# Kernel optimization log

Hardware: AMD Instinct MI355X
Metric: run time of the kernel (lower is better)

## Reference

```python
import jax, jax.numpy as jnp
import numpy as np
import itertools

# The repo's eset_ops_4_to_4 builds 69 permutation-equivariant basis ops on a
# rank-4 set tensor x[n, d, i, j, k, l]. We reconstruct the 69-dim basis as all
# order-preserving subset matchings (A, B) with A = kept input index slots,
# B = output slots receiving them (|A| = |B| = s, s = 1..4): sum x over the
# complement of A, then broadcast the reduced tensor into output positions B.
# Count: sum_{s=1..4} C(4,s)^2 = 16 + 36 + 16 + 1 = 69 (Vandermonde C(8,4)=70
# minus the s=0 global-sum term).

def _basis_pairs():
    pairs = []
    for s in range(1, 5):
        for A in itertools.combinations(range(4), s):
            for B in itertools.combinations(range(4), s):
                pairs.append((A, B))
    return pairs  # len == 69

_PAIRS = _basis_pairs()


def _forward(x, coefs, bias):
    # x: (n, d, N, N, N, N); coefs: (d, s_out, 69); bias: (1, s_out, 1,1,1,1)
    out_shape = (x.shape[0], coefs.shape[1]) + x.shape[2:]
    out = jnp.zeros(out_shape, x.dtype)
    for idx, (A, B) in enumerate(_PAIRS):
        sum_axes = tuple(2 + i for i in range(4) if i not in A)
        red = x.sum(axis=sum_axes) if sum_axes else x  # (n, d, N^|A|)
        # mix channels on the SMALL reduced tensor (op and channel mix commute)
        term = jnp.einsum('ds,nd...->ns...', coefs[:, :, idx], red)
        # place kept axes at output slots B (order-preserving), broadcast rest
        for p in range(4):
            if p not in B:
                term = jnp.expand_dims(term, axis=2 + p)
        out = out + term  # broadcasting add == broadcast then accumulate
    return out + bias


def setup_inputs() -> dict:
    key = jax.random.key(0)
    k1, k2 = jax.random.split(key)
    n, d, s_out, N, basis = 2, 8, 8, 32, 69
    x = jax.random.normal(k1, (n, d, N, N, N, N), dtype=jnp.float32)
    std = np.sqrt(2.0 / (d + s_out + basis)).astype(np.float32)
    coefs = std * jax.random.normal(k2, (d, s_out, basis), dtype=jnp.float32)
    bias = jnp.zeros((1, s_out, 1, 1, 1, 1), dtype=jnp.float32)
    return {'x': x, 'coefs': coefs, 'bias': bias}


def reference(x, coefs, bias):
    return _forward(x, coefs, bias)
```

## Files before the change

### kernel.cpp

```cpp
#include <hip/hip_runtime.h>


constexpr size_t R3SZ  = 524288;
constexpr size_t R2SZ  = 16384;
constexpr size_t R1SZ  = 512;
constexpr size_t R3OFF = 0;
constexpr size_t R2OFF = R3OFF + 4 * R3SZ;
constexpr size_t R1OFF = R2OFF + 6 * R2SZ;
constexpr size_t T2OFF = R1OFF + 4 * R1SZ;
constexpr size_t T1OFF = T2OFF + 6 * R2SZ;
constexpr size_t U3OFF = T1OFF + 4 * R1SZ;

__global__ __launch_bounds__(256) void k_plane(const float* __restrict__ x,
                                               float* __restrict__ ws) {
    __shared__ float4 cp[4][8];
    __shared__ float b012[256];
    __shared__ float b013[256];
    const int bid = blockIdx.x;
    const int jq = bid & 3;
    const int i  = (bid >> 2) & 31;
    const int nd = bid >> 7;
    const int t  = threadIdx.x;
    const int w  = t >> 6;
    const int lane = t & 63;
    const float* xp = x + ((size_t)nd << 20) + ((size_t)i << 15) + (size_t)jq * 8192;

    #pragma unroll
    for (int jj = 0; jj < 8; ++jj) {
        float4 v = *(const float4*)(xp + jj * 1024 + t * 4);
        float h = v.x + v.y + v.z + v.w;
        h += __shfl_xor(h, 1); h += __shfl_xor(h, 2); h += __shfl_xor(h, 4);
        if ((t & 7) == 0) b012[jj * 32 + (t >> 3)] = h;
        v.x += __shfl_xor(v.x, 8);  v.y += __shfl_xor(v.y, 8);
        v.z += __shfl_xor(v.z, 8);  v.w += __shfl_xor(v.w, 8);
        v.x += __shfl_xor(v.x, 16); v.y += __shfl_xor(v.y, 16);
        v.z += __shfl_xor(v.z, 16); v.w += __shfl_xor(v.w, 16);
        v.x += __shfl_xor(v.x, 32); v.y += __shfl_xor(v.y, 32);
        v.z += __shfl_xor(v.z, 32); v.w += __shfl_xor(v.w, 32);
        if (lane < 8) cp[w][lane] = v;
        __syncthreads();
        if (t < 8) {
            float4 s0 = cp[0][t], s1 = cp[1][t], s2 = cp[2][t], s3 = cp[3][t];
            float4 s;
            s.x = s0.x + s1.x + s2.x + s3.x;
            s.y = s0.y + s1.y + s2.y + s3.y;
            s.z = s0.z + s1.z + s2.z + s3.z;
            s.w = s0.w + s1.w + s2.w + s3.w;
            *(float4*)(&b013[jj * 32 + t * 4]) = s;
        }
        __syncthreads();
    }
    const size_t base = ((size_t)nd << 15) + ((size_t)i << 10) + jq * 256;
    ws[R3OFF + base + t]         = b012[t];
    ws[R3OFF + R3SZ + base + t]  = b013[t];
}

__global__ __launch_bounds__(256) void k_col(const float* __restrict__ x,
                                             float* __restrict__ ws) {
    const int b = blockIdx.x;
    const int t = threadIdx.x;
    if (b < 512) {
        const int i  = b & 31;
        const int nd = b >> 5;
        const float* xp = x + ((size_t)nd << 20) + ((size_t)i << 15) + t * 4;
        float4 acc = {0.f, 0.f, 0.f, 0.f};
        #pragma unroll 8
        for (int j = 0; j < 32; ++j) {
            float4 v = *(const float4*)(xp + j * 1024);
            acc.x += v.x; acc.y += v.y; acc.z += v.z; acc.w += v.w;
        }
        *(float4*)(ws + R3OFF + 2 * R3SZ + ((size_t)nd << 15) + ((size_t)i << 10)
                   + t * 4) = acc;
    } else {
        const int bb = b - 512;
        const int j  = bb & 31;
        const int nd = bb >> 5;
        const float* xp = x + ((size_t)nd << 20) + (size_t)j * 1024 + t * 4;
        float4 acc = {0.f, 0.f, 0.f, 0.f};
        #pragma unroll 8
        for (int i = 0; i < 32; ++i) {
            float4 v = *(const float4*)(xp + ((size_t)i << 15));
            acc.x += v.x; acc.y += v.y; acc.z += v.z; acc.w += v.w;
        }
        *(float4*)(ws + R3OFF + 3 * R3SZ + ((size_t)nd << 15) + ((size_t)j << 10)
                   + t * 4) = acc;
    }
}

__global__ __launch_bounds__(256) void k_red21(float* __restrict__ ws) {
    const int gid = blockIdx.x * 256 + threadIdx.x;
    if (gid < 98304) {
        const int b2 = gid >> 14;
        const int r  = gid & 16383;
        const int nd = r >> 10;
        const int p = (r >> 5) & 31, q = r & 31;
        const float* r012 = ws + R3OFF + ((size_t)nd << 15);
        const float* r013 = r012 + R3SZ;
        const float* r023 = r012 + 2 * R3SZ;
        float s = 0.f;
        switch (b2) {
            case 0: { const float* s0 = r012 + p * 1024 + q * 32;
                      for (int m = 0; m < 32; ++m) s += s0[m]; } break;
            case 1: { const float* s0 = r012 + p * 1024 + q;
                      for (int m = 0; m < 32; ++m) s += s0[m * 32]; } break;
            case 2: { const float* s0 = r013 + p * 1024 + q;
                      for (int m = 0; m < 32; ++m) s += s0[m * 32]; } break;
            case 3: { const float* s0 = r012 + p * 32 + q;
                      for (int m = 0; m < 32; ++m) s += s0[m * 1024]; } break;
            case 4: { const float* s0 = r013 + p * 32 + q;
                      for (int m = 0; m < 32; ++m) s += s0[m * 1024]; } break;
            default:{ const float* s0 = r023 + p * 32 + q;
                      for (int m = 0; m < 32; ++m) s += s0[m * 1024]; } break;
        }
        ws[R2OFF + (size_t)b2 * R2SZ + (size_t)nd * 1024 + p * 32 + q] = s;
    } else if (gid < 100352) {
        const int e  = gid - 98304;
        const int b1 = e >> 9;
        const int r  = e & 511;
        const int nd = r >> 5, p = r & 31;
        const float* r012 = ws + R3OFF + ((size_t)nd << 15);
        const float* r013 = r012 + R3SZ;
        float s = 0.f;
        if (b1 == 0)      { const float* s0 = r012 + p * 1024;
                            for (int m = 0; m < 1024; ++m) s += s0[m]; }
        else if (b1 == 1) { const float* s0 = r012 + p * 32;
                            for (int a = 0; a < 32; ++a) for (int m = 0; m < 32; ++m)
                                s += s0[a * 1024 + m]; }
        else if (b1 == 2) { const float* s0 = r012 + p;
                            for (int a = 0; a < 32; ++a) for (int m = 0; m < 32; ++m)
                                s += s0[a * 1024 + m * 32]; }
        else              { const float* s0 = r013 + p;
                            for (int a = 0; a < 32; ++a) for (int m = 0; m < 32; ++m)
                                s += s0[a * 1024 + m * 32]; }
        ws[R1OFF + (size_t)b1 * R1SZ + (size_t)nd * 32 + p] = s;
    }
}

__global__ __launch_bounds__(256) void k_mix21(const float* __restrict__ coefs,
                                               float* __restrict__ ws) {
    __shared__ float cs[4416];
    for (int idx = threadIdx.x; idx < 4416; idx += 256) cs[idx] = coefs[idx];
    __syncthreads();
    const int gid = blockIdx.x * 256 + threadIdx.x;
    if (gid < 98304) {
        const int b2 = gid >> 14;
        const int r  = gid & 16383;
        const int n  = r >> 13;
        const int so = (r >> 10) & 7;
        const int pq = r & 1023;
        float s = 0.f;
        #pragma unroll
        for (int a2 = 0; a2 < 6; ++a2) {
            const float* src = ws + R2OFF + (size_t)a2 * R2SZ + (size_t)(n * 8) * 1024 + pq;
            #pragma unroll
            for (int d = 0; d < 8; ++d)
                s += cs[(d * 8 + so) * 69 + 16 + a2 * 6 + b2] * src[d * 1024];
        }
        ws[T2OFF + (size_t)b2 * R2SZ + (size_t)(n * 8 + so) * 1024 + pq] = s;
    } else if (gid < 100352) {
        const int e  = gid - 98304;
        const int b1 = e >> 9;
        const int r  = e & 511;
        const int n  = r >> 8;
        const int so = (r >> 5) & 7;
        const int p  = r & 31;
        float s = 0.f;
        #pragma unroll
        for (int a1 = 0; a1 < 4; ++a1) {
            const float* src = ws + R1OFF + (size_t)a1 * R1SZ + (size_t)(n * 8) * 32 + p;
            #pragma unroll
            for (int d = 0; d < 8; ++d)
                s += cs[(d * 8 + so) * 69 + a1 * 4 + b1] * src[d * 32];
        }
        ws[T1OFF + (size_t)b1 * R1SZ + (size_t)(n * 8 + so) * 32 + p] = s;
    }
}

__global__ __launch_bounds__(256) void k_mix3(const float* __restrict__ coefs,
                                              const float* __restrict__ bias,
                                              float* __restrict__ ws) {
    __shared__ float cs[4416];
    for (int idx = threadIdx.x; idx < 4416; idx += 256) cs[idx] = coefs[idx];
    __syncthreads();
    const int blk = blockIdx.x;
    const int cb  = blk & 127;
    const int soh = (blk >> 7) & 1;
    const int n   = blk >> 8;
    const int c   = cb * 256 + threadIdx.x;
    const int p1 = c >> 10, p2 = (c >> 5) & 31, p3 = c & 31;
    float v[4][8];
    #pragma unroll
    for (int a = 0; a < 4; ++a)
        #pragma unroll
        for (int d = 0; d < 8; ++d)
            v[a][d] = ws[R3OFF + (size_t)a * R3SZ + (size_t)(n * 8 + d) * 32768 + c];
    const float* T2 = ws + T2OFF;
    const float* T1 = ws + T1OFF;
    #pragma unroll
    for (int b = 0; b < 4; ++b) {
        #pragma unroll
        for (int so2 = 0; so2 < 4; ++so2) {
            const int so = soh * 4 + so2;
            float s = 0.f;
            #pragma unroll
            for (int a = 0; a < 4; ++a)
                #pragma unroll
                for (int d = 0; d < 8; ++d)
                    s += cs[(d * 8 + so) * 69 + 52 + a * 4 + b] * v[a][d];
            const size_t nso = (size_t)(n * 8 + so);
            if (b == 0) {
                s += T2[0 * R2SZ + nso * 1024 + p1 * 32 + p2];
                s += T2[1 * R2SZ + nso * 1024 + p1 * 32 + p3];
                s += T2[3 * R2SZ + nso * 1024 + p2 * 32 + p3];
                s += T1[0 * R1SZ + nso * 32 + p1];
                s += T1[1 * R1SZ + nso * 32 + p2];
                s += T1[2 * R1SZ + nso * 32 + p3];
                s += bias[so];
            } else if (b == 1) {
                s += T2[2 * R2SZ + nso * 1024 + p1 * 32 + p3];
                s += T2[4 * R2SZ + nso * 1024 + p2 * 32 + p3];
                s += T1[3 * R1SZ + nso * 32 + p3];
            } else if (b == 2) {
                s += T2[5 * R2SZ + nso * 1024 + p2 * 32 + p3];
            }
            ws[U3OFF + (size_t)b * R3SZ + nso * 32768 + c] = s;
        }
    }
}

__global__ __launch_bounds__(256) void k_final(const float* __restrict__ x,
                                               const float* __restrict__ coefs,
                                               const float* __restrict__ ws,
                                               float* __restrict__ out) {
    __shared__ float c68[64];
    if (threadIdx.x < 64) c68[threadIdx.x] = coefs[threadIdx.x * 69 + 68];
    __syncthreads();
    const int b = blockIdx.x;
    const int j = b & 31;
    const int i = (b >> 5) & 31;
    const int n = b >> 10;
    const int t = threadIdx.x;
    const int k = t >> 3, lq = t & 7;

    float4 xv[8];
    const float* xb = x + ((size_t)n << 23) + ((size_t)i << 15) + j * 1024 + k * 32 + lq * 4;
    #pragma unroll
    for (int d = 0; d < 8; ++d) xv[d] = *(const float4*)(xb + ((size_t)d << 20));

    const float* U = ws + U3OFF;
    const size_t c012 = (size_t)i * 1024 + j * 32 + k;
    const size_t c013 = (size_t)i * 1024 + j * 32 + lq * 4;
    const size_t c023 = (size_t)i * 1024 + k * 32 + lq * 4;
    const size_t c123 = (size_t)j * 1024 + k * 32 + lq * 4;

    #pragma unroll
    for (int so = 0; so < 8; ++so) {
        const size_t nso = (size_t)(n * 8 + so) << 15;
        const float  u0 = U[0 * R3SZ + nso + c012];
        const float4 u1 = *(const float4*)(U + 1 * R3SZ + nso + c013);
        const float4 u2 = *(const float4*)(U + 2 * R3SZ + nso + c023);
        const float4 u3 = *(const float4*)(U + 3 * R3SZ + nso + c123);
        float4 acc;
        acc.x = u0 + u1.x + u2.x + u3.x;
        acc.y = u0 + u1.y + u2.y + u3.y;
        acc.z = u0 + u1.z + u2.z + u3.z;
        acc.w = u0 + u1.w + u2.w + u3.w;
        #pragma unroll
        for (int d = 0; d < 8; ++d) {
            const float w = c68[d * 8 + so];
            acc.x += w * xv[d].x; acc.y += w * xv[d].y;
            acc.z += w * xv[d].z; acc.w += w * xv[d].w;
        }
        *(float4*)(out + ((size_t)(n * 8 + so) << 20) + ((size_t)i << 15)
                   + j * 1024 + k * 32 + lq * 4) = acc;
    }
}

extern "C" void kernel_launch(void* const* d_in, const int* in_sizes, int n_in,
                              void* d_out, int out_size, void* d_ws, size_t ws_size,
                              hipStream_t stream) {
    const float* x     = (const float*)d_in[0];
    const float* coefs = (const float*)d_in[1];
    const float* bias  = (const float*)d_in[2];
    float* out = (float*)d_out;
    float* ws  = (float*)d_ws;

    hipLaunchKernelGGL(k_plane, dim3(2048), dim3(256), 0, stream, x, ws);
    hipLaunchKernelGGL(k_col,   dim3(1024), dim3(256), 0, stream, x, ws);
    hipLaunchKernelGGL(k_red21, dim3(392),  dim3(256), 0, stream, ws);
    hipLaunchKernelGGL(k_mix21, dim3(392),  dim3(256), 0, stream, coefs, ws);
    hipLaunchKernelGGL(k_mix3,  dim3(512),  dim3(256), 0, stream, coefs, bias, ws);
    hipLaunchKernelGGL(k_final, dim3(2048), dim3(256), 0, stream, x, coefs, ws, out);
}
```

Before: 203.4 us.

## Fuse plane and column reductions into one pass and fold low-rank mixing into k_mix3

Merges k_plane and the i-slab half of k_col into k_redI, so each x slab is read once to produce two rank-3, three rank-2 and three rank-1 reductions, using shuffles, shared memory and atomics. k_redJ covers the j-direction reductions and derives further rank-2 and rank-1 sums directly. The separate k_red21 and k_mix21 kernels are removed; the rank-2 and rank-1 channel mixing is recomputed per element inside k_mix3 from the reduced tensors. This removes one full read of x and two launches, but adds a memset, float atomics and redundant per-thread mixing work in k_mix3.

```diff
diff --git a/kernel.cpp b/kernel.cpp
--- a/kernel.cpp
+++ b/kernel.cpp
@@ -7,172 +7,137 @@
 constexpr size_t R3OFF = 0;
 constexpr size_t R2OFF = R3OFF + 4 * R3SZ;
 constexpr size_t R1OFF = R2OFF + 6 * R2SZ;
-constexpr size_t T2OFF = R1OFF + 4 * R1SZ;
-constexpr size_t T1OFF = T2OFF + 6 * R2SZ;
-constexpr size_t U3OFF = T1OFF + 4 * R1SZ;
-
-__global__ __launch_bounds__(256) void k_plane(const float* __restrict__ x,
-                                               float* __restrict__ ws) {
-    __shared__ float4 cp[4][8];
-    __shared__ float b012[256];
-    __shared__ float b013[256];
-    const int bid = blockIdx.x;
-    const int jq = bid & 3;
-    const int i  = (bid >> 2) & 31;
-    const int nd = bid >> 7;
+constexpr size_t U3OFF = R1OFF + 4 * R1SZ;
+
+__global__ __launch_bounds__(256) void k_redI(const float* __restrict__ x,
+                                              float* __restrict__ ws) {
+    __shared__ float  b012[1024];
+    __shared__ float4 p013[1024];
+    __shared__ float4 p03[4][8];
+    const int b  = blockIdx.x;
+    const int i  = b & 31;
+    const int nd = b >> 5;
     const int t  = threadIdx.x;
-    const int w  = t >> 6;
-    const int lane = t & 63;
-    const float* xp = x + ((size_t)nd << 20) + ((size_t)i << 15) + (size_t)jq * 8192;
-
-    #pragma unroll
-    for (int jj = 0; jj < 8; ++jj) {
-        float4 v = *(const float4*)(xp + jj * 1024 + t * 4);
+    const int lane = t & 63, w = t >> 6;
+    const int k = t >> 3, lq = t & 7;
+    const float* xp = x + ((size_t)nd << 20) + ((size_t)i << 15) + t * 4;
+
+    float4 acc = {0.f, 0.f, 0.f, 0.f};
+    #pragma unroll 8
+    for (int j = 0; j < 32; ++j) {
+        float4 v = *(const float4*)(xp + j * 1024);
+        acc.x += v.x; acc.y += v.y; acc.z += v.z; acc.w += v.w;
         float h = v.x + v.y + v.z + v.w;
         h += __shfl_xor(h, 1); h += __shfl_xor(h, 2); h += __shfl_xor(h, 4);
-        if ((t & 7) == 0) b012[jj * 32 + (t >> 3)] = h;
+        if (lq == 0) b012[j * 32 + k] = h;
         v.x += __shfl_xor(v.x, 8);  v.y += __shfl_xor(v.y, 8);
         v.z += __shfl_xor(v.z, 8);  v.w += __shfl_xor(v.w, 8);
         v.x += __shfl_xor(v.x, 16); v.y += __shfl_xor(v.y, 16);
         v.z += __shfl_xor(v.z, 16); v.w += __shfl_xor(v.w, 16);
         v.x += __shfl_xor(v.x, 32); v.y += __shfl_xor(v.y, 32);
         v.z += __shfl_xor(v.z, 32); v.w += __shfl_xor(v.w, 32);
-        if (lane < 8) cp[w][lane] = v;
-        __syncthreads();
-        if (t < 8) {
-            float4 s0 = cp[0][t], s1 = cp[1][t], s2 = cp[2][t], s3 = cp[3][t];
-            float4 s;
-            s.x = s0.x + s1.x + s2.x + s3.x;
-            s.y = s0.y + s1.y + s2.y + s3.y;
-            s.z = s0.z + s1.z + s2.z + s3.z;
-            s.w = s0.w + s1.w + s2.w + s3.w;
-            *(float4*)(&b013[jj * 32 + t * 4]) = s;
-        }
-        __syncthreads();
-    }
-    const size_t base = ((size_t)nd << 15) + ((size_t)i << 10) + jq * 256;
-    ws[R3OFF + base + t]         = b012[t];
-    ws[R3OFF + R3SZ + base + t]  = b013[t];
-}
-
-__global__ __launch_bounds__(256) void k_col(const float* __restrict__ x,
-                                             float* __restrict__ ws) {
-    const int b = blockIdx.x;
-    const int t = threadIdx.x;
-    if (b < 512) {
-        const int i  = b & 31;
-        const int nd = b >> 5;
-        const float* xp = x + ((size_t)nd << 20) + ((size_t)i << 15) + t * 4;
-        float4 acc = {0.f, 0.f, 0.f, 0.f};
-        #pragma unroll 8
-        for (int j = 0; j < 32; ++j) {
-            float4 v = *(const float4*)(xp + j * 1024);
-            acc.x += v.x; acc.y += v.y; acc.z += v.z; acc.w += v.w;
-        }
-        *(float4*)(ws + R3OFF + 2 * R3SZ + ((size_t)nd << 15) + ((size_t)i << 10)
-                   + t * 4) = acc;
-    } else {
-        const int bb = b - 512;
-        const int j  = bb & 31;
-        const int nd = bb >> 5;
-        const float* xp = x + ((size_t)nd << 20) + (size_t)j * 1024 + t * 4;
-        float4 acc = {0.f, 0.f, 0.f, 0.f};
-        #pragma unroll 8
-        for (int i = 0; i < 32; ++i) {
-            float4 v = *(const float4*)(xp + ((size_t)i << 15));
-            acc.x += v.x; acc.y += v.y; acc.z += v.z; acc.w += v.w;
-        }
-        *(float4*)(ws + R3OFF + 3 * R3SZ + ((size_t)nd << 15) + ((size_t)j << 10)
-                   + t * 4) = acc;
-    }
-}
-
-__global__ __launch_bounds__(256) void k_red21(float* __restrict__ ws) {
-    const int gid = blockIdx.x * 256 + threadIdx.x;
-    if (gid < 98304) {
-        const int b2 = gid >> 14;
-        const int r  = gid & 16383;
-        const int nd = r >> 10;
-        const int p = (r >> 5) & 31, q = r & 31;
-        const float* r012 = ws + R3OFF + ((size_t)nd << 15);
-        const float* r013 = r012 + R3SZ;
-        const float* r023 = r012 + 2 * R3SZ;
-        float s = 0.f;
-        switch (b2) {
-            case 0: { const float* s0 = r012 + p * 1024 + q * 32;
-                      for (int m = 0; m < 32; ++m) s += s0[m]; } break;
-            case 1: { const float* s0 = r012 + p * 1024 + q;
-                      for (int m = 0; m < 32; ++m) s += s0[m * 32]; } break;
-            case 2: { const float* s0 = r013 + p * 1024 + q;
-                      for (int m = 0; m < 32; ++m) s += s0[m * 32]; } break;
-            case 3: { const float* s0 = r012 + p * 32 + q;
-                      for (int m = 0; m < 32; ++m) s += s0[m * 1024]; } break;
-            case 4: { const float* s0 = r013 + p * 32 + q;
-                      for (int m = 0; m < 32; ++m) s += s0[m * 1024]; } break;
-            default:{ const float* s0 = r023 + p * 32 + q;
-                      for (int m = 0; m < 32; ++m) s += s0[m * 1024]; } break;
-        }
-        ws[R2OFF + (size_t)b2 * R2SZ + (size_t)nd * 1024 + p * 32 + q] = s;
-    } else if (gid < 100352) {
-        const int e  = gid - 98304;
-        const int b1 = e >> 9;
-        const int r  = e & 511;
-        const int nd = r >> 5, p = r & 31;
-        const float* r012 = ws + R3OFF + ((size_t)nd << 15);
-        const float* r013 = r012 + R3SZ;
-        float s = 0.f;
-        if (b1 == 0)      { const float* s0 = r012 + p * 1024;
-                            for (int m = 0; m < 1024; ++m) s += s0[m]; }
-        else if (b1 == 1) { const float* s0 = r012 + p * 32;
-                            for (int a = 0; a < 32; ++a) for (int m = 0; m < 32; ++m)
-                                s += s0[a * 1024 + m]; }
-        else if (b1 == 2) { const float* s0 = r012 + p;
-                            for (int a = 0; a < 32; ++a) for (int m = 0; m < 32; ++m)
-                                s += s0[a * 1024 + m * 32]; }
-        else              { const float* s0 = r013 + p;
-                            for (int a = 0; a < 32; ++a) for (int m = 0; m < 32; ++m)
-                                s += s0[a * 1024 + m * 32]; }
-        ws[R1OFF + (size_t)b1 * R1SZ + (size_t)nd * 32 + p] = s;
-    }
-}
-
-__global__ __launch_bounds__(256) void k_mix21(const float* __restrict__ coefs,
-                                               float* __restrict__ ws) {
-    __shared__ float cs[4416];
-    for (int idx = threadIdx.x; idx < 4416; idx += 256) cs[idx] = coefs[idx];
-    __syncthreads();
-    const int gid = blockIdx.x * 256 + threadIdx.x;
-    if (gid < 98304) {
-        const int b2 = gid >> 14;
-        const int r  = gid & 16383;
-        const int n  = r >> 13;
-        const int so = (r >> 10) & 7;
-        const int pq = r & 1023;
-        float s = 0.f;
-        #pragma unroll
-        for (int a2 = 0; a2 < 6; ++a2) {
-            const float* src = ws + R2OFF + (size_t)a2 * R2SZ + (size_t)(n * 8) * 1024 + pq;
-            #pragma unroll
-            for (int d = 0; d < 8; ++d)
-                s += cs[(d * 8 + so) * 69 + 16 + a2 * 6 + b2] * src[d * 1024];
-        }
-        ws[T2OFF + (size_t)b2 * R2SZ + (size_t)(n * 8 + so) * 1024 + pq] = s;
-    } else if (gid < 100352) {
-        const int e  = gid - 98304;
-        const int b1 = e >> 9;
-        const int r  = e & 511;
-        const int n  = r >> 8;
-        const int so = (r >> 5) & 7;
-        const int p  = r & 31;
-        float s = 0.f;
-        #pragma unroll
-        for (int a1 = 0; a1 < 4; ++a1) {
-            const float* src = ws + R1OFF + (size_t)a1 * R1SZ + (size_t)(n * 8) * 32 + p;
-            #pragma unroll
-            for (int d = 0; d < 8; ++d)
-                s += cs[(d * 8 + so) * 69 + a1 * 4 + b1] * src[d * 32];
-        }
-        ws[T1OFF + (size_t)b1 * R1SZ + (size_t)(n * 8 + so) * 32 + p] = s;
+        if (lane < 8) p013[(j * 4 + w) * 8 + lane] = v;
+    }
+    const size_t ndh = (size_t)nd << 15;
+    *(float4*)(ws + R3OFF + 2 * R3SZ + ndh + ((size_t)i << 10) + t * 4) = acc;
+    float* r23p = ws + R2OFF + 5 * R2SZ + nd * 1024 + t * 4;
+    unsafeAtomicAdd(r23p + 0, acc.x);
+    unsafeAtomicAdd(r23p + 1, acc.y);
+    unsafeAtomicAdd(r23p + 2, acc.z);
+    unsafeAtomicAdd(r23p + 3, acc.w);
+    float h2 = acc.x + acc.y + acc.z + acc.w;
+    h2 += __shfl_xor(h2, 1); h2 += __shfl_xor(h2, 2); h2 += __shfl_xor(h2, 4);
+    if (lq == 0) {
+        ws[R2OFF + 1 * R2SZ + nd * 1024 + i * 32 + k] = h2;
+        unsafeAtomicAdd(ws + R1OFF + 0 * R1SZ + nd * 32 + k, h2);
+    }
+    acc.x += __shfl_xor(acc.x, 8);  acc.y += __shfl_xor(acc.y, 8);
+    acc.z += __shfl_xor(acc.z, 8);  acc.w += __shfl_xor(acc.w, 8);
+    acc.x += __shfl_xor(acc.x, 16); acc.y += __shfl_xor(acc.y, 16);
+    acc.z += __shfl_xor(acc.z, 16); acc.w += __shfl_xor(acc.w, 16);
+    acc.x += __shfl_xor(acc.x, 32); acc.y += __shfl_xor(acc.y, 32);
+    acc.z += __shfl_xor(acc.z, 32); acc.w += __shfl_xor(acc.w, 32);
+    if (lane < 8) p03[w][lane] = acc;
+    __syncthreads();
+    *(float4*)(ws + R3OFF + ndh + ((size_t)i << 10) + t * 4) = *(float4*)(b012 + t * 4);
+    {
+        const int jj = t >> 3, ql = t & 7;
+        float4 s0 = p013[(jj * 4 + 0) * 8 + ql];
+        float4 s1 = p013[(jj * 4 + 1) * 8 + ql];
+        float4 s2 = p013[(jj * 4 + 2) * 8 + ql];
+        float4 s3 = p013[(jj * 4 + 3) * 8 + ql];
+        float4 s;
+        s.x = s0.x + s1.x + s2.x + s3.x;
+        s.y = s0.y + s1.y + s2.y + s3.y;
+        s.z = s0.z + s1.z + s2.z + s3.z;
+        s.w = s0.w + s1.w + s2.w + s3.w;
+        *(float4*)(ws + R3OFF + R3SZ + ndh + ((size_t)i << 10) + t * 4) = s;
+    }
+    if (t < 32) {
+        float ssum = 0.f;
+        #pragma unroll
+        for (int m = 0; m < 32; ++m) ssum += b012[t * 32 + ((m + t) & 31)];
+        ws[R2OFF + 0 * R2SZ + nd * 1024 + i * 32 + t] = ssum;
+    }
+    if (t < 8) {
+        float4 g0 = p03[0][t], g1 = p03[1][t], g2 = p03[2][t], g3 = p03[3][t];
+        float4 g;
+        g.x = g0.x + g1.x + g2.x + g3.x;
+        g.y = g0.y + g1.y + g2.y + g3.y;
+        g.z = g0.z + g1.z + g2.z + g3.z;
+        g.w = g0.w + g1.w + g2.w + g3.w;
+        *(float4*)(ws + R2OFF + 2 * R2SZ + nd * 1024 + i * 32 + t * 4) = g;
+        float* r3p = ws + R1OFF + 1 * R1SZ + nd * 32 + t * 4;
+        unsafeAtomicAdd(r3p + 0, g.x);
+        unsafeAtomicAdd(r3p + 1, g.y);
+        unsafeAtomicAdd(r3p + 2, g.z);
+        unsafeAtomicAdd(r3p + 3, g.w);
+        float gs = g.x + g.y + g.z + g.w;
+        gs += __shfl_xor(gs, 1); gs += __shfl_xor(gs, 2); gs += __shfl_xor(gs, 4);
+        if (t == 0) ws[R1OFF + 2 * R1SZ + nd * 32 + i] = gs;
+    }
+}
+
+__global__ __launch_bounds__(256) void k_redJ(const float* __restrict__ x,
+                                              float* __restrict__ ws) {
+    __shared__ float4 p13[4][8];
+    const int b  = blockIdx.x;
+    const int j  = b & 31;
+    const int nd = b >> 5;
+    const int t  = threadIdx.x;
+    const int lane = t & 63, w = t >> 6;
+    const int k = t >> 3, lq = t & 7;
+    const float* xp = x + ((size_t)nd << 20) + ((size_t)j << 10) + t * 4;
+
+    float4 acc = {0.f, 0.f, 0.f, 0.f};
+    #pragma unroll 8
+    for (int i = 0; i < 32; ++i) {
+        float4 v = *(const float4*)(xp + ((size_t)i << 15));
+        acc.x += v.x; acc.y += v.y; acc.z += v.z; acc.w += v.w;
+    }
+    *(float4*)(ws + R3OFF + 3 * R3SZ + ((size_t)nd << 15) + ((size_t)j << 10) + t * 4) = acc;
+    float h = acc.x + acc.y + acc.z + acc.w;
+    h += __shfl_xor(h, 1); h += __shfl_xor(h, 2); h += __shfl_xor(h, 4);
+    if (lq == 0) ws[R2OFF + 3 * R2SZ + nd * 1024 + j * 32 + k] = h;
+    acc.x += __shfl_xor(acc.x, 8);  acc.y += __shfl_xor(acc.y, 8);
+    acc.z += __shfl_xor(acc.z, 8);  acc.w += __shfl_xor(acc.w, 8);
+    acc.x += __shfl_xor(acc.x, 16); acc.y += __shfl_xor(acc.y, 16);
+    acc.z += __shfl_xor(acc.z, 16); acc.w += __shfl_xor(acc.w, 16);
+    acc.x += __shfl_xor(acc.x, 32); acc.y += __shfl_xor(acc.y, 32);
+    acc.z += __shfl_xor(acc.z, 32); acc.w += __shfl_xor(acc.w, 32);
+    if (lane < 8) p13[w][lane] = acc;
+    __syncthreads();
+    if (t < 8) {
+        float4 g0 = p13[0][t], g1 = p13[1][t], g2 = p13[2][t], g3 = p13[3][t];
+        float4 g;
+        g.x = g0.x + g1.x + g2.x + g3.x;
+        g.y = g0.y + g1.y + g2.y + g3.y;
+        g.z = g0.z + g1.z + g2.z + g3.z;
+        g.w = g0.w + g1.w + g2.w + g3.w;
+        *(float4*)(ws + R2OFF + 4 * R2SZ + nd * 1024 + j * 32 + t * 4) = g;
+        float gs = g.x + g.y + g.z + g.w;
+        gs += __shfl_xor(gs, 1); gs += __shfl_xor(gs, 2); gs += __shfl_xor(gs, 4);
+        if (t == 0) ws[R1OFF + 3 * R1SZ + nd * 32 + j] = gs;
     }
 }
 
@@ -180,7 +145,9 @@
                                               const float* __restrict__ bias,
                                               float* __restrict__ ws) {
     __shared__ float cs[4416];
+    __shared__ float bs[8];
     for (int idx = threadIdx.x; idx < 4416; idx += 256) cs[idx] = coefs[idx];
+    if (threadIdx.x < 8) bs[threadIdx.x] = bias[threadIdx.x];
     __syncthreads();
     const int blk = blockIdx.x;
     const int cb  = blk & 127;
@@ -188,42 +155,75 @@
     const int n   = blk >> 8;
     const int c   = cb * 256 + threadIdx.x;
     const int p1 = c >> 10, p2 = (c >> 5) & 31, p3 = c & 31;
+    const int q01 = p1 * 32 + p2, qA = p1 * 32 + p3, qB = p2 * 32 + p3;
+    const int nd0 = n * 8;
+
+    float t2[6][4] = {{0.f}};
+    #pragma unroll
+    for (int a2 = 0; a2 < 6; ++a2) {
+        const float* r2a = ws + R2OFF + (size_t)a2 * R2SZ + (size_t)nd0 * 1024;
+        #pragma unroll
+        for (int d = 0; d < 8; ++d) {
+            const float* rr = r2a + d * 1024;
+            const float v01 = rr[q01], vA = rr[qA], vB = rr[qB];
+            const float* cc = cs + (d * 8 + soh * 4) * 69 + 16 + a2 * 6;
+            #pragma unroll
+            for (int s = 0; s < 4; ++s) {
+                const float* c2 = cc + s * 69;
+                t2[0][s] += c2[0] * v01;
+                t2[1][s] += c2[1] * vA;
+                t2[2][s] += c2[2] * vA;
+                t2[3][s] += c2[3] * vB;
+                t2[4][s] += c2[4] * vB;
+                t2[5][s] += c2[5] * vB;
+            }
+        }
+    }
+    float t1[4][4] = {{0.f}};
+    #pragma unroll
+    for (int a1 = 0; a1 < 4; ++a1) {
+        const float* r1a = ws + R1OFF + (size_t)((a1 + 2) & 3) * R1SZ + (size_t)nd0 * 32;
+        #pragma unroll
+        for (int d = 0; d < 8; ++d) {
+            const float* rr = r1a + d * 32;
+            const float u1 = rr[p1], u2 = rr[p2], u3 = rr[p3];
+            const float* cc = cs + (d * 8 + soh * 4) * 69 + a1 * 4;
+            #pragma unroll
+            for (int s = 0; s < 4; ++s) {
+                const float* c1 = cc + s * 69;
+                t1[0][s] += c1[0] * u1;
+                t1[1][s] += c1[1] * u2;
+                t1[2][s] += c1[2] * u3;
+                t1[3][s] += c1[3] * u3;
+            }
+        }
+    }
     float v[4][8];
     #pragma unroll
     for (int a = 0; a < 4; ++a)
         #pragma unroll
         for (int d = 0; d < 8; ++d)
-            v[a][d] = ws[R3OFF + (size_t)a * R3SZ + (size_t)(n * 8 + d) * 32768 + c];
-    const float* T2 = ws + T2OFF;
-    const float* T1 = ws + T1OFF;
+            v[a][d] = ws[R3OFF + (size_t)a * R3SZ + (size_t)(nd0 + d) * 32768 + c];
     #pragma unroll
     for (int b = 0; b < 4; ++b) {
         #pragma unroll
-        for (int so2 = 0; so2 < 4; ++so2) {
-            const int so = soh * 4 + so2;
-            float s = 0.f;
+        for (int s = 0; s < 4; ++s) {
+            const int so = soh * 4 + s;
+            float sum = 0.f;
             #pragma unroll
             for (int a = 0; a < 4; ++a)
                 #pragma unroll
                 for (int d = 0; d < 8; ++d)
-                    s += cs[(d * 8 + so) * 69 + 52 + a * 4 + b] * v[a][d];
-            const size_t nso = (size_t)(n * 8 + so);
+                    sum += cs[(d * 8 + so) * 69 + 52 + a * 4 + b] * v[a][d];
             if (b == 0) {
-                s += T2[0 * R2SZ + nso * 1024 + p1 * 32 + p2];
-                s += T2[1 * R2SZ + nso * 1024 + p1 * 32 + p3];
-                s += T2[3 * R2SZ + nso * 1024 + p2 * 32 + p3];
-                s += T1[0 * R1SZ + nso * 32 + p1];
-                s += T1[1 * R1SZ + nso * 32 + p2];
-                s += T1[2 * R1SZ + nso * 32 + p3];
-                s += bias[so];
+                sum += t2[0][s] + t2[1][s] + t2[3][s]
+                     + t1[0][s] + t1[1][s] + t1[2][s] + bs[so];
             } else if (b == 1) {
-                s += T2[2 * R2SZ + nso * 1024 + p1 * 32 + p3];
-                s += T2[4 * R2SZ + nso * 1024 + p2 * 32 + p3];
-                s += T1[3 * R1SZ + nso * 32 + p3];
+                sum += t2[2][s] + t2[4][s] + t1[3][s];
             } else if (b == 2) {
-                s += T2[5 * R2SZ + nso * 1024 + p2 * 32 + p3];
+                sum += t2[5][s];
             }
-            ws[U3OFF + (size_t)b * R3SZ + nso * 32768 + c] = s;
+            ws[U3OFF + (size_t)b * R3SZ + (size_t)(nd0 + so) * 32768 + c] = sum;
         }
     }
 }
@@ -285,10 +285,10 @@
     float* out = (float*)d_out;
     float* ws  = (float*)d_ws;
 
-    hipLaunchKernelGGL(k_plane, dim3(2048), dim3(256), 0, stream, x, ws);
-    hipLaunchKernelGGL(k_col,   dim3(1024), dim3(256), 0, stream, x, ws);
-    hipLaunchKernelGGL(k_red21, dim3(392),  dim3(256), 0, stream, ws);
-    hipLaunchKernelGGL(k_mix21, dim3(392),  dim3(256), 0, stream, coefs, ws);
+    hipMemsetAsync(ws + R2OFF + 5 * R2SZ, 0, 17408 * sizeof(float), stream);
+
+    hipLaunchKernelGGL(k_redI,  dim3(512),  dim3(256), 0, stream, x, ws);
+    hipLaunchKernelGGL(k_redJ,  dim3(512),  dim3(256), 0, stream, x, ws);
     hipLaunchKernelGGL(k_mix3,  dim3(512),  dim3(256), 0, stream, coefs, bias, ws);
     hipLaunchKernelGGL(k_final, dim3(2048), dim3(256), 0, stream, x, coefs, ws, out);
 }
```

Result: slower. 217.1 us (+6.7%).
